# Kernel tuning notes

Hardware: AMD Instinct MI355X
Metric: run time of the kernel (lower is better)

Reference implementation:

```python
import jax, jax.numpy as jnp
import numpy as np

ALPHA = 0.2  # LeakyReLU negative slope
EPS = 1e-8


def setup_inputs() -> dict:
    key = jax.random.key(0)
    ks = jax.random.split(key, 7)
    N, Fin, Fout, E = 100000, 256, 128, 800000
    node_embedding = jax.random.normal(ks[0], (N, Fin), dtype=jnp.float32)
    adj_pos = jax.random.randint(ks[1], (2, E), 0, N, dtype=jnp.int64)
    adj_neg = jax.random.randint(ks[2], (2, E), 0, N, dtype=jnp.int64)
    edge_embedding = jax.random.normal(ks[3], (2, Fout), dtype=jnp.float32)
    Wr = jax.random.normal(ks[4], (2, Fin, Fout), dtype=jnp.float32) * 0.05
    a = jax.random.normal(ks[5], (1, 2 * Fout), dtype=jnp.float32) * 0.05
    bias = jax.random.normal(ks[6], (1, Fout), dtype=jnp.float32) * 0.05
    return dict(node_embedding=node_embedding, edge_embedding=edge_embedding,
                Wr=Wr, a=a, bias=bias, adj_pos=adj_pos, adj_neg=adj_neg)


def reference(node_embedding, edge_embedding, Wr, a, bias, adj_pos, adj_neg):
    N = node_embedding.shape[0]
    Fout = Wr.shape[2]
    # h_r = X @ Wr[r], then column-scale by edge_embedding[r] (== mm with diag)
    h_pos = (node_embedding @ Wr[0]) * edge_embedding[0]  # [N, Fout]
    h_neg = (node_embedding @ Wr[1]) * edge_embedding[1]  # [N, Fout]
    a_src = a[0, :Fout]  # attention weights for source half of concat
    a_dst = a[0, Fout:]  # attention weights for dest half

    def edge_scores(h, adj):
        # a . [h[src], h[dst]] computed as node-level dots then scalar gather
        s = h @ a_src  # [N]
        d = h @ a_dst  # [N]
        z = s[adj[0]] + d[adj[1]]  # [E]
        z = jnp.where(z > 0, z, ALPHA * z)  # LeakyReLU
        return jax.nn.sigmoid(z)

    e_pos = edge_scores(h_pos, adj_pos)  # [E_pos]
    e_neg = edge_scores(h_neg, adj_neg)  # [E_neg]

    # row-sum normalizer: spmm(edge, edge_e, ones) == segment_sum over row idx
    rows = jnp.concatenate([adj_pos[0], adj_neg[0]])
    e_all = jnp.concatenate([e_pos, e_neg])
    row_sum = jax.ops.segment_sum(e_all, rows, num_segments=N) + EPS  # [N]

    # weighted aggregation: out[i] = sum_{(i,j)} e_ij * h[j]
    agg = (jax.ops.segment_sum(e_pos[:, None] * h_pos[adj_pos[1]], adj_pos[0], num_segments=N)
           + jax.ops.segment_sum(e_neg[:, None] * h_neg[adj_neg[1]], adj_neg[0], num_segments=N))
    return agg / row_sum[:, None] + bias
```

## Files before the change

### kernel.cpp

```cpp
#include <hip/hip_runtime.h>

#define ALPHA 0.2f
#define EPSV 1e-8f
#define BUCK_BITS 8
#define BUCK (1 << BUCK_BITS)
#define CAP 5120
#define EPB_A 4096
#define EPT_A (EPB_A / 256)

typedef float f32x4 __attribute__((ext_vector_type(4)));
typedef short bf16x8 __attribute__((ext_vector_type(8)));

static __device__ __forceinline__ unsigned short f2bf(float f) {
    union { float f; unsigned int u; } c; c.f = f;
    unsigned int u = c.u;
    unsigned int round = ((u >> 16) & 1) + 0x7FFF;
    return (unsigned short)((u + round) >> 16);
}
static __device__ __forceinline__ float bflo(unsigned int u) {
    union { unsigned int u; float f; } c; c.u = u << 16; return c.f;
}
static __device__ __forceinline__ float bfhi(unsigned int u) {
    union { unsigned int u; float f; } c; c.u = u & 0xFFFF0000u; return c.f;
}

__global__ __launch_bounds__(256) void convB_binA_kernel(
    const float* __restrict__ Wr, uint4* __restrict__ Bp,
    const int* __restrict__ adj_pos, const int* __restrict__ adj_neg,
    int* __restrict__ bucketCount, unsigned int* __restrict__ edges_tmp,
    int N, int E)
{
    __shared__ int hist[512];
    __shared__ int base[512];
    __shared__ int cur[512];
    const int tid = threadIdx.x;

    if ((int)blockIdx.x < 32) {
        const int t = blockIdx.x * 256 + tid;
        const int kb  = t >> 8;
        const int col = t & 255;
        const int rel = col >> 7;
        const int cc  = col & 127;
        unsigned short v[8];
        #pragma unroll
        for (int jj = 0; jj < 8; ++jj) {
            const int k = kb * 8 + jj;
            v[jj] = f2bf(Wr[(size_t)rel * 256 * 128 + (size_t)k * 128 + cc]);
        }
        Bp[t] = *reinterpret_cast<const uint4*>(v);
        return;
    }

    const int bb = blockIdx.x - 32;
    const long long e0 = (long long)bb * EPB_A;
    const long long twoE = 2LL * E;

    hist[tid] = 0;
    hist[tid + 256] = 0;

    int esrc[EPT_A];
    unsigned int erec[EPT_A];
    #pragma unroll
    for (int k = 0; k < EPT_A; ++k) {
        const long long idx = e0 + (long long)k * 256 + tid;
        if (idx < twoE) {
            const int rel = (idx >= E) ? 1 : 0;
            const long long eidx = rel ? idx - E : idx;
            const int* __restrict__ adj = rel ? adj_neg : adj_pos;
            const int src = adj[eidx];
            const int dst = adj[E + eidx];
            esrc[k] = src;
            erec[k] = (unsigned int)dst | ((unsigned int)rel << 17) |
                      ((unsigned int)(src & (BUCK - 1)) << 18);
        } else {
            esrc[k] = -1;
        }
    }
    __syncthreads();

    #pragma unroll
    for (int k = 0; k < EPT_A; ++k)
        if (esrc[k] >= 0) atomicAdd(&hist[esrc[k] >> BUCK_BITS], 1);
    __syncthreads();

    {
        const int rot = (bb * 61) & 511;
        #pragma unroll
        for (int q = 0; q < 2; ++q) {
            const int t2 = (tid + q * 256 + rot) & 511;
            const int hv = hist[t2];
            base[t2] = hv ? atomicAdd(&bucketCount[t2], hv) : 0;
            cur[t2] = 0;
        }
    }
    __syncthreads();

    #pragma unroll
    for (int k = 0; k < EPT_A; ++k) {
        if (esrc[k] >= 0) {
            const int b = esrc[k] >> BUCK_BITS;
            const int r = atomicAdd(&cur[b], 1);
            const int pos = base[b] + r;
            if (pos < CAP)
                edges_tmp[(size_t)b * CAP + pos] = erec[k];
        }
    }
}

__global__ __launch_bounds__(256) void mfma_gemm_kernel(
    const float* __restrict__ X, const uint4* __restrict__ Bp,
    const float* __restrict__ ee, const float* __restrict__ a,
    unsigned int* __restrict__ h32, float* __restrict__ sd, int N)
{
    __shared__ unsigned short Alds[32 * 256];
    const int tid  = threadIdx.x;
    const int lane = tid & 63;
    const int w    = tid >> 6;
    const int wm   = w >> 1;
    const int wn   = w & 1;
    const int cl   = lane & 15;
    const int g    = lane >> 4;
    const int tile0 = blockIdx.x * 32;

    {
        float4 fa[4], fb[4];
        #pragma unroll
        for (int pass = 0; pass < 4; ++pass) {
            const int L  = pass * 256 + tid;
            const int r  = L >> 5;
            const int c8 = L & 31;
            const int row = tile0 + r;
            fa[pass] = make_float4(0.f, 0.f, 0.f, 0.f);
            fb[pass] = make_float4(0.f, 0.f, 0.f, 0.f);
            if (row < N) {
                const float* xp = &X[(size_t)row * 256 + c8 * 8];
                fa[pass] = *reinterpret_cast<const float4*>(xp);
                fb[pass] = *reinterpret_cast<const float4*>(xp + 4);
            }
        }
        #pragma unroll
        for (int pass = 0; pass < 4; ++pass) {
            const int L  = pass * 256 + tid;
            const int r  = L >> 5;
            const int c8 = L & 31;
            unsigned short v[8];
            v[0]=f2bf(fa[pass].x); v[1]=f2bf(fa[pass].y);
            v[2]=f2bf(fa[pass].z); v[3]=f2bf(fa[pass].w);
            v[4]=f2bf(fb[pass].x); v[5]=f2bf(fb[pass].y);
            v[6]=f2bf(fb[pass].z); v[7]=f2bf(fb[pass].w);
            const int su = c8 ^ (r & 7);
            *reinterpret_cast<bf16x8*>(&Alds[r * 256 + su * 8]) =
                *reinterpret_cast<const bf16x8*>(v);
        }
    }
    __syncthreads();

    f32x4 acc[8];
    #pragma unroll
    for (int ct = 0; ct < 8; ++ct)
        acc[ct] = (f32x4){0.f, 0.f, 0.f, 0.f};

    const int rl = wm * 16 + cl;
    bf16x8 bcur[8], acur;
    {
        const int ku = g;
        #pragma unroll
        for (int ct = 0; ct < 8; ++ct) {
            const int col = wn * 128 + ct * 16 + cl;
            bcur[ct] = *reinterpret_cast<const bf16x8*>(Bp + ku * 256 + col);
        }
        acur = *reinterpret_cast<const bf16x8*>(
            &Alds[rl * 256 + (ku ^ (rl & 7)) * 8]);
    }
    #pragma unroll
    for (int kc = 0; kc < 8; ++kc) {
        bf16x8 bnext[8], anext;
        if (kc < 7) {
            const int ku = (kc + 1) * 4 + g;
            #pragma unroll
            for (int ct = 0; ct < 8; ++ct) {
                const int col = wn * 128 + ct * 16 + cl;
                bnext[ct] = *reinterpret_cast<const bf16x8*>(Bp + ku * 256 + col);
            }
            anext = *reinterpret_cast<const bf16x8*>(
                &Alds[rl * 256 + (ku ^ (rl & 7)) * 8]);
        }
        #pragma unroll
        for (int ct = 0; ct < 8; ++ct)
            acc[ct] = __builtin_amdgcn_mfma_f32_16x16x32_bf16(
                acur, bcur[ct], acc[ct], 0, 0, 0);
        if (kc < 7) {
            #pragma unroll
            for (int ct = 0; ct < 8; ++ct) bcur[ct] = bnext[ct];
            acur = anext;
        }
    }

    const int rt = blockIdx.x * 2 + wm;
    float eev[8], asv[8], adv[8];
    #pragma unroll
    for (int ct = 0; ct < 8; ++ct) {
        const int col = wn * 128 + ct * 16 + cl;
        const int cc  = col & 127;
        eev[ct] = ee[col];
        asv[ct] = a[cc];
        adv[ct] = a[128 + cc];
    }

    float s_acc[4], d_acc[4];
    #pragma unroll
    for (int reg = 0; reg < 4; ++reg) {
        const int row = rt * 16 + g * 4 + reg;
        const bool ok = row < N;
        float sp = 0.f, dp = 0.f;
        float vv[8];
        #pragma unroll
        for (int ct = 0; ct < 8; ++ct) {
            vv[ct] = acc[ct][reg] * eev[ct];
            sp += vv[ct] * asv[ct];
            dp += vv[ct] * adv[ct];
        }
        if (ok) {
            #pragma unroll
            for (int q = 0; q < 4; ++q) {
                const unsigned int u =
                    (unsigned int)f2bf(vv[2 * q]) |
                    ((unsigned int)f2bf(vv[2 * q + 1]) << 16);
                h32[((size_t)wn * N + row) * 64 + q * 16 + cl] = u;
            }
        }
        s_acc[reg] = sp;
        d_acc[reg] = dp;
    }
    #pragma unroll
    for (int reg = 0; reg < 4; ++reg) {
        float sp = s_acc[reg], dp = d_acc[reg];
        #pragma unroll
        for (int off = 1; off < 16; off <<= 1) {
            sp += __shfl_xor(sp, off);
            dp += __shfl_xor(dp, off);
        }
        if (cl == 0) {
            const int row = rt * 16 + g * 4 + reg;
            if (row < N) {
                sd[(size_t)wn * 2 * N + row]     = sp;
                sd[(size_t)wn * 2 * N + N + row] = dp;
            }
        }
    }
}

__global__ __launch_bounds__(512) void sortB_kernel(
    const int* __restrict__ bucketCount, const unsigned int* __restrict__ edges_tmp,
    const float* __restrict__ sd,
    uint2* __restrict__ edges_final,
    int* __restrict__ rowBeg, int* __restrict__ rowEnd,
    float* __restrict__ rowSum, int N)
{
    __shared__ int hist[BUCK];
    __shared__ int cur[BUCK];
    __shared__ int ssum[BUCK];
    __shared__ float sSrc[2][BUCK];
    __shared__ float rsLds[BUCK];
    const int tid = threadIdx.x;
    const int b   = blockIdx.x;
    const int s0  = b << BUCK_BITS;
    const size_t tb = (size_t)b * CAP;
    const int cnt = min(bucketCount[b], CAP);

    if (tid < BUCK) {
        hist[tid] = 0;
        rsLds[tid] = 0.f;
        const int gsrc = s0 + tid;
        sSrc[0][tid] = (gsrc < N) ? sd[gsrc] : 0.f;
        sSrc[1][tid] = (gsrc < N) ? sd[2 * (size_t)N + gsrc] : 0.f;
    }
    __syncthreads();
    for (int j = tid; j < cnt; j += 512)
        atomicAdd(&hist[edges_tmp[tb + j] >> 18], 1);
    __syncthreads();

    int h0 = 0, incl = 0;
    if (tid < BUCK) { h0 = hist[tid]; ssum[tid] = h0; incl = h0; }
    __syncthreads();
    for (int off = 1; off < BUCK; off <<= 1) {
        const int u = (tid < BUCK && tid >= off) ? ssum[tid - off] : 0;
        __syncthreads();
        if (tid < BUCK) { incl += u; ssum[tid] = incl; }
        __syncthreads();
    }
    if (tid < BUCK) {
        const int excl = incl - h0;
        cur[tid] = excl;
        const int gidx = s0 + tid;
        if (gidx < N) {
            rowBeg[gidx] = (int)tb + excl;
            rowEnd[gidx] = (int)tb + incl;
        }
    }
    __syncthreads();
    for (int j = tid; j < cnt; j += 512) {
        const unsigned int r = edges_tmp[tb + j];
        const int sl  = r >> 18;
        const int rel = (r >> 17) & 1;
        const int dst = r & 0x1FFFF;
        float z = sSrc[rel][sl] + sd[(size_t)rel * 2 * N + N + dst];
        z = z > 0.f ? z : ALPHA * z;
        const float ev = 1.f / (1.f + __expf(-z));
        const int pos = atomicAdd(&cur[sl], 1);
        atomicAdd(&rsLds[sl], ev);
        edges_final[tb + pos] =
            make_uint2((unsigned int)(rel * N + dst), __float_as_uint(ev));
    }
    __syncthreads();
    if (tid < BUCK) {
        const int gidx = s0 + tid;
        if (gidx < N) rowSum[gidx] = rsLds[tid];
    }
}

__global__ __launch_bounds__(256) void gather_kernel(
    const int* __restrict__ rowBeg, const int* __restrict__ rowEnd,
    const float* __restrict__ rowSum,
    const uint2* __restrict__ edges,
    const unsigned int* __restrict__ h32,
    const float* __restrict__ bias, float* __restrict__ out, int N)
{
    const long long gw = ((long long)blockIdx.x * blockDim.x + threadIdx.x) >> 6;
    const int lane = threadIdx.x & 63;
    if (gw >= N) return;
    const int n = (int)gw;

    const int beg = rowBeg[n];
    const int end = rowEnd[n];
    const unsigned loff = (unsigned)(lane << 2);
    const char* __restrict__ hb = (const char*)h32;

    float ax = 0.f, ay = 0.f;
    int j = beg;
    for (; j + 8 <= end; j += 8) {
        uint2 r[8];
        #pragma unroll
        for (int k = 0; k < 8; ++k) r[k] = edges[j + k];
        unsigned int hv[8];
        #pragma unroll
        for (int k = 0; k < 8; ++k)
            hv[k] = *reinterpret_cast<const unsigned int*>(
                hb + ((r[k].x << 8) + loff));
        #pragma unroll
        for (int k = 0; k < 8; ++k) {
            const float e = __uint_as_float(r[k].y);
            ax += e * bflo(hv[k]);
            ay += e * bfhi(hv[k]);
        }
    }
    for (; j + 4 <= end; j += 4) {
        uint2 r[4];
        #pragma unroll
        for (int k = 0; k < 4; ++k) r[k] = edges[j + k];
        unsigned int hv[4];
        #pragma unroll
        for (int k = 0; k < 4; ++k)
            hv[k] = *reinterpret_cast<const unsigned int*>(
                hb + ((r[k].x << 8) + loff));
        #pragma unroll
        for (int k = 0; k < 4; ++k) {
            const float e = __uint_as_float(r[k].y);
            ax += e * bflo(hv[k]);
            ay += e * bfhi(hv[k]);
        }
    }
    for (; j < end; ++j) {
        const uint2 r = edges[j];
        const unsigned int hv = *reinterpret_cast<const unsigned int*>(
            hb + ((r.x << 8) + loff));
        const float e = __uint_as_float(r.y);
        ax += e * bflo(hv);
        ay += e * bfhi(hv);
    }
    const float inv = 1.f / (rowSum[n] + EPSV);
    const int q  = lane >> 4;
    const int cl = lane & 15;
    const int c0 = q * 32 + cl;
    const int c1 = c0 + 16;
    out[(size_t)n * 128 + c0] = ax * inv + bias[c0];
    out[(size_t)n * 128 + c1] = ay * inv + bias[c1];
}

extern "C" void kernel_launch(void* const* d_in, const int* in_sizes, int n_in,
                              void* d_out, int out_size, void* d_ws, size_t ws_size,
                              hipStream_t stream) {
    const float* X      = (const float*)d_in[0];
    const float* ee     = (const float*)d_in[1];
    const float* Wr     = (const float*)d_in[2];
    const float* a      = (const float*)d_in[3];
    const float* bias   = (const float*)d_in[4];
    const int* adj_pos  = (const int*)d_in[5];
    const int* adj_neg  = (const int*)d_in[6];

    const int N = in_sizes[0] / 256;
    const int E = in_sizes[5] / 2;
    const int twoE = 2 * E;
    float* out = (float*)d_out;

    const int gemmBlocks = (N + 31) / 32;
    const int NBUCK = (N + BUCK - 1) >> BUCK_BITS;
    const int binBlocks = (twoE + EPB_A - 1) / EPB_A;

    char* ws = (char*)d_ws;
    uint4* Bp = (uint4*)ws;
    char* p = ws + 32 * 256 * 16;
    unsigned int* h32 = (unsigned int*)p; p += (size_t)2 * N * 64 * 4;
    float* sd         = (float*)p;  p += (size_t)4 * N * 4;
    int* bucketCount  = (int*)p;    p += 512 * 4;
    int* rowBeg       = (int*)p;    p += (size_t)N * 4;
    int* rowEnd       = (int*)p;    p += (size_t)N * 4;
    float* rowSum     = (float*)p;  p += (size_t)N * 4;
    p = (char*)(((uintptr_t)p + 15) & ~(uintptr_t)15);
    unsigned int* edges_tmp = (unsigned int*)p; p += (size_t)NBUCK * CAP * 4;
    uint2* edges_final = (uint2*)p; p += (size_t)NBUCK * CAP * 8;

    (void)hipMemsetAsync(bucketCount, 0, 512 * sizeof(int), stream);

    convB_binA_kernel<<<32 + binBlocks, 256, 0, stream>>>(
        Wr, Bp, adj_pos, adj_neg, bucketCount, edges_tmp, N, E);

    mfma_gemm_kernel<<<gemmBlocks, 256, 0, stream>>>(X, Bp, ee, a, h32, sd, N);

    sortB_kernel<<<NBUCK, 512, 0, stream>>>(
        bucketCount, edges_tmp, sd, edges_final, rowBeg, rowEnd, rowSum, N);

    gather_kernel<<<(int)(((long long)N * 64 + 255) / 256), 256, 0, stream>>>(
        rowBeg, rowEnd, rowSum, edges_final, h32, bias, out, N);
}
```

Measured before the change: 171.4 us.

## Split GEMM K-loop in halves to overlap second-half X loads with MFMAs

The GEMM kernel now stages the X tile into shared memory in two K-halves. The first half is loaded, converted and stored before the sync. The second half's global loads are issued into registers and held in flight while the MFMAs for the first half run, then converted and stored after them. The explicit register double-buffering of B fragments is removed in favour of a simple per-chunk load. This aims to hide global-load latency of the X tile behind compute, at the cost of an extra barrier and of no longer prefetching B fragments one step ahead.

```diff
diff --git a/kernel.cpp b/kernel.cpp
--- a/kernel.cpp
+++ b/kernel.cpp
@@ -122,38 +122,43 @@
     const int g    = lane >> 4;
     const int tile0 = blockIdx.x * 32;
 
-    {
-        float4 fa[4], fb[4];
-        #pragma unroll
-        for (int pass = 0; pass < 4; ++pass) {
-            const int L  = pass * 256 + tid;
-            const int r  = L >> 5;
-            const int c8 = L & 31;
-            const int row = tile0 + r;
-            fa[pass] = make_float4(0.f, 0.f, 0.f, 0.f);
-            fb[pass] = make_float4(0.f, 0.f, 0.f, 0.f);
-            if (row < N) {
-                const float* xp = &X[(size_t)row * 256 + c8 * 8];
-                fa[pass] = *reinterpret_cast<const float4*>(xp);
-                fb[pass] = *reinterpret_cast<const float4*>(xp + 4);
-            }
-        }
-        #pragma unroll
-        for (int pass = 0; pass < 4; ++pass) {
-            const int L  = pass * 256 + tid;
-            const int r  = L >> 5;
-            const int c8 = L & 31;
-            unsigned short v[8];
-            v[0]=f2bf(fa[pass].x); v[1]=f2bf(fa[pass].y);
-            v[2]=f2bf(fa[pass].z); v[3]=f2bf(fa[pass].w);
-            v[4]=f2bf(fb[pass].x); v[5]=f2bf(fb[pass].y);
-            v[6]=f2bf(fb[pass].z); v[7]=f2bf(fb[pass].w);
-            const int su = c8 ^ (r & 7);
-            *reinterpret_cast<bf16x8*>(&Alds[r * 256 + su * 8]) =
-                *reinterpret_cast<const bf16x8*>(v);
-        }
-    }
-    __syncthreads();
+    #pragma unroll
+    for (int pass = 0; pass < 2; ++pass) {
+        const int L  = pass * 256 + tid;
+        const int r  = L >> 4;
+        const int c8 = L & 15;
+        const int row = tile0 + r;
+        float4 f0 = make_float4(0.f, 0.f, 0.f, 0.f);
+        float4 f1 = make_float4(0.f, 0.f, 0.f, 0.f);
+        if (row < N) {
+            const float* xp = &X[(size_t)row * 256 + c8 * 8];
+            f0 = *reinterpret_cast<const float4*>(xp);
+            f1 = *reinterpret_cast<const float4*>(xp + 4);
+        }
+        unsigned short v[8];
+        v[0]=f2bf(f0.x); v[1]=f2bf(f0.y); v[2]=f2bf(f0.z); v[3]=f2bf(f0.w);
+        v[4]=f2bf(f1.x); v[5]=f2bf(f1.y); v[6]=f2bf(f1.z); v[7]=f2bf(f1.w);
+        const int su = c8 ^ (r & 7);
+        *reinterpret_cast<bf16x8*>(&Alds[r * 256 + su * 8]) =
+            *reinterpret_cast<const bf16x8*>(v);
+    }
+    __syncthreads();
+
+    float4 g0[2], g1[2];
+    #pragma unroll
+    for (int pass = 0; pass < 2; ++pass) {
+        const int L  = pass * 256 + tid;
+        const int r  = L >> 4;
+        const int c8 = L & 15;
+        const int row = tile0 + r;
+        g0[pass] = make_float4(0.f, 0.f, 0.f, 0.f);
+        g1[pass] = make_float4(0.f, 0.f, 0.f, 0.f);
+        if (row < N) {
+            const float* xp = &X[(size_t)row * 256 + 128 + c8 * 8];
+            g0[pass] = *reinterpret_cast<const float4*>(xp);
+            g1[pass] = *reinterpret_cast<const float4*>(xp + 4);
+        }
+    }
 
     f32x4 acc[8];
     #pragma unroll
@@ -161,39 +166,54 @@
         acc[ct] = (f32x4){0.f, 0.f, 0.f, 0.f};
 
     const int rl = wm * 16 + cl;
-    bf16x8 bcur[8], acur;
-    {
-        const int ku = g;
+    #pragma unroll
+    for (int kc = 0; kc < 4; ++kc) {
+        const int ku = kc * 4 + g;
+        const bf16x8 af = *reinterpret_cast<const bf16x8*>(
+            &Alds[rl * 256 + (ku ^ (rl & 7)) * 8]);
+        bf16x8 bfr[8];
         #pragma unroll
         for (int ct = 0; ct < 8; ++ct) {
             const int col = wn * 128 + ct * 16 + cl;
-            bcur[ct] = *reinterpret_cast<const bf16x8*>(Bp + ku * 256 + col);
-        }
-        acur = *reinterpret_cast<const bf16x8*>(
-            &Alds[rl * 256 + (ku ^ (rl & 7)) * 8]);
-    }
-    #pragma unroll
-    for (int kc = 0; kc < 8; ++kc) {
-        bf16x8 bnext[8], anext;
-        if (kc < 7) {
-            const int ku = (kc + 1) * 4 + g;
-            #pragma unroll
-            for (int ct = 0; ct < 8; ++ct) {
-                const int col = wn * 128 + ct * 16 + cl;
-                bnext[ct] = *reinterpret_cast<const bf16x8*>(Bp + ku * 256 + col);
-            }
-            anext = *reinterpret_cast<const bf16x8*>(
-                &Alds[rl * 256 + (ku ^ (rl & 7)) * 8]);
+            bfr[ct] = *reinterpret_cast<const bf16x8*>(Bp + ku * 256 + col);
         }
         #pragma unroll
         for (int ct = 0; ct < 8; ++ct)
             acc[ct] = __builtin_amdgcn_mfma_f32_16x16x32_bf16(
-                acur, bcur[ct], acc[ct], 0, 0, 0);
-        if (kc < 7) {
-            #pragma unroll
-            for (int ct = 0; ct < 8; ++ct) bcur[ct] = bnext[ct];
-            acur = anext;
-        }
+                af, bfr[ct], acc[ct], 0, 0, 0);
+    }
+
+    #pragma unroll
+    for (int pass = 0; pass < 2; ++pass) {
+        const int L  = pass * 256 + tid;
+        const int r  = L >> 4;
+        const int c8 = L & 15;
+        unsigned short v[8];
+        v[0]=f2bf(g0[pass].x); v[1]=f2bf(g0[pass].y);
+        v[2]=f2bf(g0[pass].z); v[3]=f2bf(g0[pass].w);
+        v[4]=f2bf(g1[pass].x); v[5]=f2bf(g1[pass].y);
+        v[6]=f2bf(g1[pass].z); v[7]=f2bf(g1[pass].w);
+        const int su = (16 + c8) ^ (r & 7);
+        *reinterpret_cast<bf16x8*>(&Alds[r * 256 + su * 8]) =
+            *reinterpret_cast<const bf16x8*>(v);
+    }
+    __syncthreads();
+
+    #pragma unroll
+    for (int kc = 4; kc < 8; ++kc) {
+        const int ku = kc * 4 + g;
+        const bf16x8 af = *reinterpret_cast<const bf16x8*>(
+            &Alds[rl * 256 + (ku ^ (rl & 7)) * 8]);
+        bf16x8 bfr[8];
+        #pragma unroll
+        for (int ct = 0; ct < 8; ++ct) {
+            const int col = wn * 128 + ct * 16 + cl;
+            bfr[ct] = *reinterpret_cast<const bf16x8*>(Bp + ku * 256 + col);
+        }
+        #pragma unroll
+        for (int ct = 0; ct < 8; ++ct)
+            acc[ct] = __builtin_amdgcn_mfma_f32_16x16x32_bf16(
+                af, bfr[ct], acc[ct], 0, 0, 0);
     }
 
     const int rt = blockIdx.x * 2 + wm;
```

New measurement: 170.4 us. About the same (-0.6%).
